# Kernel optimization log

Hardware: AMD Instinct MI355X
Metric: run time of the kernel (lower is better)

## Reference

```python
import jax, jax.numpy as jnp
import numpy as np

S, B, D = 1024, 2, 1024      # seq, batch, embed_dim
E, TOPK = 15, 3              # routed experts = 8*2-1, top_n = 2*2-1
F = 1024                     # per-expert ffn dim (ffn_dim // m)
FS = 2048                    # shared expert ffn dim (ffn_dim * n_shared)


def _uinit(k, shape, out_dim):
    std = out_dim ** -0.5
    return jax.random.uniform(k, shape, jnp.float32, -std, std)


def setup_inputs() -> dict:
    key = jax.random.key(0)
    ks = jax.random.split(key, 10)
    return {
        "x": jax.random.normal(ks[0], (S, B, D), jnp.float32),
        "gate_w": jax.random.normal(ks[1], (E, D), jnp.float32) * (D ** -0.5),
        "fc1_w": _uinit(ks[2], (E, 2 * F, D), 2 * F),
        "fc1_b": _uinit(ks[3], (E, 2 * F), 2 * F),
        "geglu_mult": jnp.ones((E, F), jnp.float32),
        "fc2_w": _uinit(ks[4], (E, D, F), D),
        "fc2_b": _uinit(ks[5], (E, D), D),
        "s_fc1_w": _uinit(ks[6], (2 * FS, D), 2 * FS),
        "s_fc1_b": _uinit(ks[7], (2 * FS,), 2 * FS),
        "s_geglu_mult": jnp.ones((FS,), jnp.float32),
        "s_fc2_w": _uinit(ks[8], (D, FS), D),
        "s_fc2_b": _uinit(ks[9], (D,), D),
    }


def reference(x, gate_w, fc1_w, fc1_b, geglu_mult, fc2_w, fc2_b,
              s_fc1_w, s_fc1_b, s_geglu_mult, s_fc2_w, s_fc2_b):
    s, b, d = x.shape
    xt = x.reshape(-1, d)                              # [T, D] tokens
    T = xt.shape[0]

    # --- gate: softmax over routed experts, top-k, renormalize ---
    logits = xt @ gate_w.T                             # [T, E]
    scores = jax.nn.softmax(logits, axis=-1)
    topk_w, topk_idx = jax.lax.top_k(scores, TOPK)     # [T, K]
    topk_w = topk_w / (jnp.sum(topk_w, axis=-1, keepdims=True) + 1e-20)
    # combine weights: zero for non-routed experts (same math as dispatch/scatter)
    comb = jnp.zeros((T, E), xt.dtype).at[jnp.arange(T)[:, None], topk_idx].add(topk_w)

    # --- routed experts: GEGLU FFN applied as grouped GEMM, weighted combine ---
    h = jnp.einsum('td,efd->etf', xt, fc1_w) + fc1_b[:, None, :]   # [E, T, 2F]
    xh, g = h[..., :F], h[..., F:]                                 # chunk: (x, gate)
    a = jax.nn.gelu(g, approximate=False) * xh * geglu_mult[:, None, :]
    yexp = jnp.einsum('etf,edf->etd', a, fc2_w) + fc2_b[:, None, :]  # [E, T, D]
    y = jnp.einsum('etd,te->td', yexp, comb)                         # [T, D]

    # --- shared expert ---
    hs = xt @ s_fc1_w.T + s_fc1_b                      # [T, 2*FS]
    xs, gs = hs[..., :FS], hs[..., FS:]
    as_ = jax.nn.gelu(gs, approximate=False) * xs * s_geglu_mult
    ys = as_ @ s_fc2_w.T + s_fc2_b                     # [T, D]

    return (y + ys).reshape(s, b, d)
```

## Files before the change

### kernel.cpp

```cpp
#include <hip/hip_runtime.h>

typedef __attribute__((ext_vector_type(8))) short bfrag;
typedef __attribute__((ext_vector_type(4))) float f32x4;

__device__ __forceinline__ short f2bf(float f) {
  union { float f; unsigned u; } v; v.f = f;
  unsigned r = v.u + 0x7FFFu + ((v.u >> 16) & 1u);
  return (short)(r >> 16);
}
__device__ __forceinline__ float bf2f(unsigned short h) {
  union { unsigned u; float f; } v; v.u = ((unsigned)h) << 16;
  return v.f;
}
__device__ __forceinline__ float gelu_exact(float g) {
  return 0.5f * g * (1.0f + erff(g * 0.70710678118654752f));
}
__device__ __forceinline__ void gld_lds16(const short* g, short* l) {
  __builtin_amdgcn_global_load_lds(
      (const __attribute__((address_space(1))) void*)g,
      (__attribute__((address_space(3))) void*)l, 16, 0, 0);
}

__global__ __launch_bounds__(256) void k_convert_w(
    const float* __restrict__ s0, const float* __restrict__ s1,
    const float* __restrict__ s2, const float* __restrict__ s3,
    short* __restrict__ d0, short* __restrict__ d1,
    short* __restrict__ d2, short* __restrict__ d3)
{
  const int b = blockIdx.x;
  const float* s; short* d; long off;
  if (b < 3840)      { s = s0; d = d0; off = (long)b * 2048; }
  else if (b < 5760) { s = s1; d = d1; off = (long)(b - 3840) * 2048; }
  else if (b < 6272) { s = s2; d = d2; off = (long)(b - 5760) * 2048; }
  else               { s = s3; d = d3; off = (long)(b - 6272) * 2048; }
  const f32x4* sp = (const f32x4*)s;
  const long i0 = off + threadIdx.x;
  f32x4 v[8];
#pragma unroll
  for (int j = 0; j < 8; j++) v[j] = __builtin_nontemporal_load(sp + i0 + j * 256);
#pragma unroll
  for (int j = 0; j < 8; j++)
    ((short4*)d)[i0 + j * 256] =
        make_short4(f2bf(v[j].x), f2bf(v[j].y), f2bf(v[j].z), f2bf(v[j].w));
}

__global__ __launch_bounds__(64) void k_gate(const float* __restrict__ x,
    const float* __restrict__ gw, int* __restrict__ topk_idx,
    float* __restrict__ topk_w, short* __restrict__ xbf)
{
  const int t0 = blockIdx.x * 4;
  const int lane = threadIdx.x;
  float xv[4][16];
#pragma unroll
  for (int tt = 0; tt < 4; tt++)
#pragma unroll
    for (int i = 0; i < 16; i++) {
      xv[tt][i] = x[(size_t)(t0 + tt) * 1024 + lane + 64 * i];
      xbf[(size_t)(t0 + tt) * 1024 + lane + 64 * i] = f2bf(xv[tt][i]);
    }
  float p[4][15];
#pragma unroll
  for (int e = 0; e < 15; e++) {
    float wv[16];
#pragma unroll
    for (int i = 0; i < 16; i++) wv[i] = gw[(size_t)e * 1024 + lane + 64 * i];
#pragma unroll
    for (int tt = 0; tt < 4; tt++) {
      float s = 0.f;
#pragma unroll
      for (int i = 0; i < 16; i++) s += xv[tt][i] * wv[i];
#pragma unroll
      for (int o = 32; o; o >>= 1) s += __shfl_xor(s, o, 64);
      p[tt][e] = s;
    }
  }
#pragma unroll
  for (int tt = 0; tt < 4; tt++) {
    float m = -1e30f;
#pragma unroll
    for (int e = 0; e < 15; e++) m = fmaxf(m, p[tt][e]);
    float q[15], Z = 0.f;
#pragma unroll
    for (int e = 0; e < 15; e++) { q[e] = expf(p[tt][e] - m); Z += q[e]; }
    int usedMask = 0; int bi[3]; float bv[3];
#pragma unroll
    for (int j = 0; j < 3; j++) {
      float best = -1.f; int b = 0;
#pragma unroll
      for (int e = 0; e < 15; e++) {
        bool ok = (!((usedMask >> e) & 1)) && (q[e] > best);
        if (ok) { best = q[e]; b = e; }
      }
      bi[j] = b; bv[j] = best / Z; usedMask |= 1 << b;
    }
    if (lane == tt) {
      float den = bv[0] + bv[1] + bv[2] + 1e-20f;
#pragma unroll
      for (int j = 0; j < 3; j++) {
        topk_idx[(t0 + tt) * 3 + j] = bi[j];
        topk_w[(t0 + tt) * 3 + j] = bv[j] / den;
      }
    }
  }
}

__global__ __launch_bounds__(1024) void k_route(const int* __restrict__ topk_idx,
    const float* __restrict__ topk_w, int* __restrict__ cnt_g, int* __restrict__ offs_g,
    int* __restrict__ row_tok, float* __restrict__ row_wt, int* __restrict__ row_id)
{
  __shared__ int scnt[16], soffs[16], sfill[16];
  const int tid = threadIdx.x;
  if (tid < 16) { scnt[tid] = 0; sfill[tid] = 0; }
  __syncthreads();
  for (int i = tid; i < 6144; i += 1024) atomicAdd(&scnt[topk_idx[i]], 1);
  __syncthreads();
  if (tid == 0) {
    int a = 0;
    for (int e = 0; e < 15; e++) { soffs[e] = a; offs_g[e] = a; cnt_g[e] = scnt[e]; a += scnt[e]; }
  }
  __syncthreads();
  for (int i = tid; i < 6144; i += 1024) {
    int e = topk_idx[i];
    int pos = atomicAdd(&sfill[e], 1);
    int row = soffs[e] + pos;
    row_tok[row] = i / 3;
    row_wt[row] = topk_w[i];
    row_id[i] = row;
  }
}

__device__ __forceinline__ bool resolve_tile256(const int* __restrict__ cnt, int ty,
                                                int& e, int& lt) {
  int acc = 0;
#pragma unroll
  for (int i = 0; i < 15; i++) {
    int tl = (cnt[i] + 255) >> 8;
    if (ty < acc + tl) { e = i; lt = ty - acc; return true; }
    acc += tl;
  }
  return false;
}

__global__ __launch_bounds__(512, 2) void k_fc1(
    const short* __restrict__ xbf,
    const short* __restrict__ wsh, const float* __restrict__ bsh, const float* __restrict__ msh,
    const short* __restrict__ wex, const float* __restrict__ bex, const float* __restrict__ mex,
    const int* __restrict__ cnt, const int* __restrict__ offs, const int* __restrict__ row_tok,
    short* __restrict__ as_buf, short* __restrict__ a_buf)
{
  __shared__ short smem[2 * 32768];
  const int tid = threadIdx.x;
  const int bid = blockIdx.x;
  const bool sh = bid < 128;
  int f0, m0 = 0, e = 0, rowBase = 0, nrows = 256;
  if (sh) {
    f0 = (bid & 15) * 128; m0 = (bid >> 4) * 256;
  } else {
    const int b2 = bid - 128;
    int lt;
    if (!resolve_tile256(cnt, b2 >> 3, e, lt)) return;
    f0 = (b2 & 7) * 128;
    rowBase = offs[e] + lt * 256;
    nrows = cnt[e] - lt * 256; if (nrows > 256) nrows = 256;
  }
  const int lane = tid & 63, ml = lane & 15, kq = lane >> 4, mlo = lane & 7;
  const int wv = tid >> 6, wr = wv >> 2, wc = wv & 3;
  const int lrow = lane >> 3, lchk = lane & 7;
  const int Fhalf = sh ? 2048 : 1024;
  const short* wptr = sh ? wsh : (wex + (size_t)e * 2048 * 1024);
  const short* aSrc[4]; const short* bSrc[4];
#pragma unroll
  for (int t = 0; t < 4; t++) {
    const int r = wv * 32 + t * 8 + lrow;
    const int sc = (lchk ^ (r & 7)) * 8;
    if (sh) aSrc[t] = xbf + (size_t)(m0 + r) * 1024 + sc;
    else {
      const int rc = r < nrows ? r : nrows - 1;
      aSrc[t] = xbf + (size_t)row_tok[rowBase + rc] * 1024 + sc;
    }
    const int grow = (r < 128) ? (f0 + r) : (Fhalf + f0 + r - 128);
    bSrc[t] = wptr + (size_t)grow * 1024 + sc;
  }
  f32x4 acc[8][4] = {};

#define FC1_STAGE(BUF, K0) do {                                              \
    short* A_ = smem + (BUF) * 32768;                                        \
    short* B_ = A_ + 16384;                                                  \
    _Pragma("unroll")                                                        \
    for (int t = 0; t < 4; t++) gld_lds16(aSrc[t] + (K0), A_ + (wv * 32 + t * 8) * 64); \
    _Pragma("unroll")                                                        \
    for (int t = 0; t < 4; t++) gld_lds16(bSrc[t] + (K0), B_ + (wv * 32 + t * 8) * 64); \
  } while (0)

#define FC1_COMPUTE(BUF) do {                                                \
    const short* As_ = smem + (BUF) * 32768;                                 \
    const short* Bs_ = As_ + 16384;                                          \
    _Pragma("unroll")                                                        \
    for (int kk = 0; kk < 2; kk++) {                                         \
      const int so = ((kk * 4 + kq) ^ mlo) * 8;                              \
      bfrag af[8], bb[4];                                                    \
      _Pragma("unroll")                                                      \
      for (int i = 0; i < 8; i++)                                            \
        af[i] = *(const bfrag*)&As_[(wr * 128 + i * 16 + ml) * 64 + so];     \
      _Pragma("unroll")                                                      \
      for (int j = 0; j < 4; j++) {                                          \
        const int brow = (j >> 1) * 128 + wc * 32 + (j & 1) * 16 + ml;       \
        bb[j] = *(const bfrag*)&Bs_[brow * 64 + so];                         \
      }                                                                      \
      _Pragma("unroll")                                                      \
      for (int i = 0; i < 8; i++)                                            \
        _Pragma("unroll")                                                    \
        for (int j = 0; j < 4; j++)                                          \
          acc[i][j] = __builtin_amdgcn_mfma_f32_16x16x32_bf16(af[i], bb[j], acc[i][j], 0, 0, 0); \
    }                                                                        \
  } while (0)

  FC1_STAGE(0, 0);
  __syncthreads();
  int cur = 0;
  for (int ks = 0; ks < 15; ks++) {
    FC1_STAGE(cur ^ 1, (ks + 1) * 64);
    FC1_COMPUTE(cur);
    __syncthreads();
    cur ^= 1;
  }
  FC1_COMPUTE(cur);

  const float* bias = sh ? bsh : (bex + (size_t)e * 2048);
  const float* mult = sh ? msh : (mex + (size_t)e * 1024);
#pragma unroll
  for (int jj = 0; jj < 2; jj++) {
    const int fl = wc * 32 + jj * 16 + ml;
    const int f = f0 + fl;
    const float b1 = bias[f];
    const float b2 = bias[Fhalf + f];
    const float mv = mult[f];
#pragma unroll
    for (int i = 0; i < 8; i++)
#pragma unroll
      for (int rg = 0; rg < 4; rg++) {
        const int row = wr * 128 + i * 16 + kq * 4 + rg;
        const float h1 = acc[i][jj][rg] + b1;
        const float h2 = acc[i][jj + 2][rg] + b2;
        const short o = f2bf(gelu_exact(h2) * h1 * mv);
        if (sh) as_buf[(size_t)(m0 + row) * 2048 + f] = o;
        else if (row < nrows) a_buf[(size_t)(rowBase + row) * 1024 + f] = o;
      }
  }
}

__global__ __launch_bounds__(512, 2) void k_fc2(
    const short* __restrict__ as_buf, const short* __restrict__ wsfc2, const float* __restrict__ s_b,
    const short* __restrict__ a_buf, const short* __restrict__ wfc2, const float* __restrict__ e_b,
    const int* __restrict__ cnt, const int* __restrict__ offs, const float* __restrict__ row_wt,
    float* __restrict__ y, short* __restrict__ yexp)
{
  __shared__ short smem[2 * 24576];
  const int tid = threadIdx.x;
  const int bid = blockIdx.x;
  const bool sh = bid < 64;
  int d0, m0 = 0, e = 0, rowBase = 0, nrows = 256, Klen, astr, bstr;
  const short *aBase, *bBase;
  if (sh) {
    d0 = (bid & 7) * 128; m0 = (bid >> 3) * 256;
    Klen = 2048; astr = 2048; bstr = 2048;
    aBase = as_buf; bBase = wsfc2;
  } else {
    const int b2 = bid - 64;
    int lt;
    if (!resolve_tile256(cnt, b2 >> 3, e, lt)) return;
    d0 = (b2 & 7) * 128;
    rowBase = offs[e] + lt * 256;
    nrows = cnt[e] - lt * 256; if (nrows > 256) nrows = 256;
    Klen = 1024; astr = 1024; bstr = 1024;
    aBase = a_buf + (size_t)rowBase * 1024;
    bBase = wfc2 + (size_t)e * 1024 * 1024;
  }
  const int lane = tid & 63, ml = lane & 15, kq = lane >> 4, mlo = lane & 7;
  const int wv = tid >> 6, wr = wv >> 2, wc = wv & 3;
  const int lrow = lane >> 3, lchk = lane & 7;
  const short* aSrc[4]; const short* bSrc[2];
#pragma unroll
  for (int t = 0; t < 4; t++) {
    const int r = wv * 32 + t * 8 + lrow;
    const int sc = (lchk ^ (r & 7)) * 8;
    const int rc = (sh || r < nrows) ? r : nrows - 1;
    aSrc[t] = aBase + (size_t)(sh ? (m0 + r) : rc) * astr + sc;
  }
#pragma unroll
  for (int t = 0; t < 2; t++) {
    const int rb = wv * 16 + t * 8 + lrow;
    const int sc = (lchk ^ (rb & 7)) * 8;
    bSrc[t] = bBase + (size_t)(d0 + rb) * bstr + sc;
  }
  f32x4 acc[8][2] = {};

#define FC2_STAGE(BUF, K0) do {                                              \
    short* A_ = smem + (BUF) * 24576;                                        \
    short* B_ = A_ + 16384;                                                  \
    _Pragma("unroll")                                                        \
    for (int t = 0; t < 4; t++) gld_lds16(aSrc[t] + (K0), A_ + (wv * 32 + t * 8) * 64); \
    _Pragma("unroll")                                                        \
    for (int t = 0; t < 2; t++) gld_lds16(bSrc[t] + (K0), B_ + (wv * 16 + t * 8) * 64); \
  } while (0)

#define FC2_COMPUTE(BUF) do {                                                \
    const short* As_ = smem + (BUF) * 24576;                                 \
    const short* Bs_ = As_ + 16384;                                          \
    _Pragma("unroll")                                                        \
    for (int kk = 0; kk < 2; kk++) {                                         \
      const int so = ((kk * 4 + kq) ^ mlo) * 8;                              \
      bfrag af[8], bb[2];                                                    \
      _Pragma("unroll")                                                      \
      for (int i = 0; i < 8; i++)                                            \
        af[i] = *(const bfrag*)&As_[(wr * 128 + i * 16 + ml) * 64 + so];     \
      _Pragma("unroll")                                                      \
      for (int j = 0; j < 2; j++)                                            \
        bb[j] = *(const bfrag*)&Bs_[(wc * 32 + j * 16 + ml) * 64 + so];      \
      _Pragma("unroll")                                                      \
      for (int i = 0; i < 8; i++)                                            \
        _Pragma("unroll")                                                    \
        for (int j = 0; j < 2; j++)                                          \
          acc[i][j] = __builtin_amdgcn_mfma_f32_16x16x32_bf16(af[i], bb[j], acc[i][j], 0, 0, 0); \
    }                                                                        \
  } while (0)

  FC2_STAGE(0, 0);
  __syncthreads();
  int cur = 0;
  const int NK = Klen >> 6;
  for (int ks = 0; ks < NK - 1; ks++) {
    FC2_STAGE(cur ^ 1, (ks + 1) * 64);
    FC2_COMPUTE(cur);
    __syncthreads();
    cur ^= 1;
  }
  FC2_COMPUTE(cur);

#pragma unroll
  for (int j = 0; j < 2; j++) {
    const int d = d0 + wc * 32 + j * 16 + ml;
    const float bv = sh ? s_b[d] : e_b[(size_t)e * 1024 + d];
#pragma unroll
    for (int i = 0; i < 8; i++)
#pragma unroll
      for (int rg = 0; rg < 4; rg++) {
        const int row = wr * 128 + i * 16 + kq * 4 + rg;
        if (sh) {
          y[(size_t)(m0 + row) * 1024 + d] = acc[i][j][rg] + bv;
        } else if (row < nrows) {
          const float wt = row_wt[rowBase + row];
          yexp[(size_t)(rowBase + row) * 1024 + d] = f2bf((acc[i][j][rg] + bv) * wt);
        }
      }
  }
}

__global__ __launch_bounds__(256) void k_combine(float* __restrict__ y,
    const short* __restrict__ yexp, const int* __restrict__ row_id)
{
  const int idx = blockIdx.x * 256 + threadIdx.x;
  const int t = idx >> 8;
  const int d4 = (idx & 255) * 4;
  const int r0 = row_id[t * 3], r1 = row_id[t * 3 + 1], r2 = row_id[t * 3 + 2];
  float4 acc = *(float4*)(y + (size_t)t * 1024 + d4);
  const ushort4 v0 = *(const ushort4*)(yexp + (size_t)r0 * 1024 + d4);
  const ushort4 v1 = *(const ushort4*)(yexp + (size_t)r1 * 1024 + d4);
  const ushort4 v2 = *(const ushort4*)(yexp + (size_t)r2 * 1024 + d4);
  acc.x += bf2f(v0.x) + bf2f(v1.x) + bf2f(v2.x);
  acc.y += bf2f(v0.y) + bf2f(v1.y) + bf2f(v2.y);
  acc.z += bf2f(v0.z) + bf2f(v1.z) + bf2f(v2.z);
  acc.w += bf2f(v0.w) + bf2f(v1.w) + bf2f(v2.w);
  *(float4*)(y + (size_t)t * 1024 + d4) = acc;
}

extern "C" void kernel_launch(void* const* d_in, const int* in_sizes, int n_in,
                              void* d_out, int out_size, void* d_ws, size_t ws_size,
                              hipStream_t stream) {
  const float* x          = (const float*)d_in[0];
  const float* gate_w     = (const float*)d_in[1];
  const float* fc1_w      = (const float*)d_in[2];
  const float* fc1_b      = (const float*)d_in[3];
  const float* geglu_mult = (const float*)d_in[4];
  const float* fc2_w      = (const float*)d_in[5];
  const float* fc2_b      = (const float*)d_in[6];
  const float* s_fc1_w    = (const float*)d_in[7];
  const float* s_fc1_b    = (const float*)d_in[8];
  const float* s_mult     = (const float*)d_in[9];
  const float* s_fc2_w    = (const float*)d_in[10];
  const float* s_fc2_b    = (const float*)d_in[11];
  float* y = (float*)d_out;

  char* wsb = (char*)d_ws;
  int*   cnt      = (int*)(wsb + 0);
  int*   offs     = (int*)(wsb + 64);
  int*   topk_idx = (int*)(wsb + 256);
  float* topk_w   = (float*)(wsb + 24832);
  int*   row_tok  = (int*)(wsb + 49408);
  float* row_wt   = (float*)(wsb + 74496);
  int*   row_id   = (int*)(wsb + 99584);
  short* xbf      = (short*)(wsb + 131072);
  short* a_buf    = (short*)(wsb + 8519680);
  short* as_buf   = (short*)(wsb + 21364736);
  short* yexp     = (short*)(wsb + 29753344);
  short* wbf_sfc1 = (short*)(wsb + 42598400);
  short* wbf_sfc2 = (short*)(wsb + 50987008);
  short* wbf_fc1  = (short*)(wsb + 55181312);
  short* wbf_fc2  = (short*)(wsb + 118095872);

  k_convert_w<<<6528, 256, 0, stream>>>(fc1_w, fc2_w, s_fc1_w, s_fc2_w,
                                        wbf_fc1, wbf_fc2, wbf_sfc1, wbf_sfc2);
  k_gate<<<512, 64, 0, stream>>>(x, gate_w, topk_idx, topk_w, xbf);
  k_route<<<1, 1024, 0, stream>>>(topk_idx, topk_w, cnt, offs, row_tok, row_wt, row_id);
  k_fc1<<<440, 512, 0, stream>>>(xbf, wbf_sfc1, s_fc1_b, s_mult,
                                 wbf_fc1, fc1_b, geglu_mult,
                                 cnt, offs, row_tok, as_buf, a_buf);
  k_fc2<<<376, 512, 0, stream>>>(as_buf, wbf_sfc2, s_fc2_b,
                                 a_buf, wbf_fc2, fc2_b,
                                 cnt, offs, row_wt, y, yexp);
  k_combine<<<2048, 256, 0, stream>>>(y, yexp, row_id);
}
```

Measured before the change: 416.7 us.

## Use 4-stage BK=32 LDS pipeline with vmcnt waits in fc1/fc2 GEMMs

Both grouped-GEMM kernels change from a double-buffered K=64 tile with a full __syncthreads per step to a four-buffer ring of K=32 tiles with three stages in flight. Waits use explicit s_waitcnt vmcnt counts plus a raw s_barrier, and sched_barrier separates the load issue from the MFMA block. The LDS swizzle is redone for 32-wide rows. The aim is to hide global-to-LDS latency better at the same LDS footprint, at the cost of twice as many barriers and hand-tuned vmcnt values that must match the number of outstanding loads.

```diff
diff --git a/kernel.cpp b/kernel.cpp
--- a/kernel.cpp
+++ b/kernel.cpp
@@ -148,7 +148,7 @@
     const int* __restrict__ cnt, const int* __restrict__ offs, const int* __restrict__ row_tok,
     short* __restrict__ as_buf, short* __restrict__ a_buf)
 {
-  __shared__ short smem[2 * 32768];
+  __shared__ short smem[4 * 16384];
   const int tid = threadIdx.x;
   const int bid = blockIdx.x;
   const bool sh = bid < 128;
@@ -163,68 +163,69 @@
     rowBase = offs[e] + lt * 256;
     nrows = cnt[e] - lt * 256; if (nrows > 256) nrows = 256;
   }
-  const int lane = tid & 63, ml = lane & 15, kq = lane >> 4, mlo = lane & 7;
+  const int lane = tid & 63, ml = lane & 15, kq = lane >> 4;
   const int wv = tid >> 6, wr = wv >> 2, wc = wv & 3;
-  const int lrow = lane >> 3, lchk = lane & 7;
+  const int scol = ((lane & 3) ^ (((lane >> 2) ^ (lane >> 4)) & 3)) * 8;
+  const int so = (kq ^ ((ml ^ (ml >> 2)) & 3)) * 8;
   const int Fhalf = sh ? 2048 : 1024;
   const short* wptr = sh ? wsh : (wex + (size_t)e * 2048 * 1024);
-  const short* aSrc[4]; const short* bSrc[4];
-#pragma unroll
-  for (int t = 0; t < 4; t++) {
-    const int r = wv * 32 + t * 8 + lrow;
-    const int sc = (lchk ^ (r & 7)) * 8;
-    if (sh) aSrc[t] = xbf + (size_t)(m0 + r) * 1024 + sc;
+  const short* aSrc[2]; const short* bSrc[2];
+#pragma unroll
+  for (int t = 0; t < 2; t++) {
+    const int r = wv * 32 + t * 16 + (lane >> 2);
+    if (sh) aSrc[t] = xbf + (size_t)(m0 + r) * 1024 + scol;
     else {
       const int rc = r < nrows ? r : nrows - 1;
-      aSrc[t] = xbf + (size_t)row_tok[rowBase + rc] * 1024 + sc;
+      aSrc[t] = xbf + (size_t)row_tok[rowBase + rc] * 1024 + scol;
     }
     const int grow = (r < 128) ? (f0 + r) : (Fhalf + f0 + r - 128);
-    bSrc[t] = wptr + (size_t)grow * 1024 + sc;
+    bSrc[t] = wptr + (size_t)grow * 1024 + scol;
   }
   f32x4 acc[8][4] = {};
 
 #define FC1_STAGE(BUF, K0) do {                                              \
-    short* A_ = smem + (BUF) * 32768;                                        \
-    short* B_ = A_ + 16384;                                                  \
-    _Pragma("unroll")                                                        \
-    for (int t = 0; t < 4; t++) gld_lds16(aSrc[t] + (K0), A_ + (wv * 32 + t * 8) * 64); \
-    _Pragma("unroll")                                                        \
-    for (int t = 0; t < 4; t++) gld_lds16(bSrc[t] + (K0), B_ + (wv * 32 + t * 8) * 64); \
+    short* A_ = smem + (BUF) * 16384;                                        \
+    short* B_ = A_ + 8192;                                                   \
+    _Pragma("unroll")                                                        \
+    for (int t = 0; t < 2; t++)                                              \
+      gld_lds16(aSrc[t] + (K0), A_ + (wv * 32 + t * 16) * 32);               \
+    _Pragma("unroll")                                                        \
+    for (int t = 0; t < 2; t++)                                              \
+      gld_lds16(bSrc[t] + (K0), B_ + (wv * 32 + t * 16) * 32);               \
   } while (0)
 
 #define FC1_COMPUTE(BUF) do {                                                \
-    const short* As_ = smem + (BUF) * 32768;                                 \
-    const short* Bs_ = As_ + 16384;                                          \
-    _Pragma("unroll")                                                        \
-    for (int kk = 0; kk < 2; kk++) {                                         \
-      const int so = ((kk * 4 + kq) ^ mlo) * 8;                              \
-      bfrag af[8], bb[4];                                                    \
+    const short* As_ = smem + (BUF) * 16384;                                 \
+    const short* Bs_ = As_ + 8192;                                           \
+    bfrag af[8], bb[4];                                                      \
+    _Pragma("unroll")                                                        \
+    for (int i = 0; i < 8; i++)                                              \
+      af[i] = *(const bfrag*)&As_[(wr * 128 + i * 16 + ml) * 32 + so];       \
+    _Pragma("unroll")                                                        \
+    for (int j = 0; j < 4; j++) {                                            \
+      const int brow = (j >> 1) * 128 + wc * 32 + (j & 1) * 16 + ml;         \
+      bb[j] = *(const bfrag*)&Bs_[brow * 32 + so];                           \
+    }                                                                        \
+    _Pragma("unroll")                                                        \
+    for (int i = 0; i < 8; i++)                                              \
       _Pragma("unroll")                                                      \
-      for (int i = 0; i < 8; i++)                                            \
-        af[i] = *(const bfrag*)&As_[(wr * 128 + i * 16 + ml) * 64 + so];     \
-      _Pragma("unroll")                                                      \
-      for (int j = 0; j < 4; j++) {                                          \
-        const int brow = (j >> 1) * 128 + wc * 32 + (j & 1) * 16 + ml;       \
-        bb[j] = *(const bfrag*)&Bs_[brow * 64 + so];                         \
-      }                                                                      \
-      _Pragma("unroll")                                                      \
-      for (int i = 0; i < 8; i++)                                            \
-        _Pragma("unroll")                                                    \
-        for (int j = 0; j < 4; j++)                                          \
-          acc[i][j] = __builtin_amdgcn_mfma_f32_16x16x32_bf16(af[i], bb[j], acc[i][j], 0, 0, 0); \
-    }                                                                        \
+      for (int j = 0; j < 4; j++)                                            \
+        acc[i][j] = __builtin_amdgcn_mfma_f32_16x16x32_bf16(af[i], bb[j], acc[i][j], 0, 0, 0); \
   } while (0)
 
   FC1_STAGE(0, 0);
-  __syncthreads();
-  int cur = 0;
-  for (int ks = 0; ks < 15; ks++) {
-    FC1_STAGE(cur ^ 1, (ks + 1) * 64);
-    FC1_COMPUTE(cur);
-    __syncthreads();
-    cur ^= 1;
-  }
-  FC1_COMPUTE(cur);
+  FC1_STAGE(1, 32);
+  FC1_STAGE(2, 64);
+  for (int ks = 0; ks < 32; ks++) {
+    if (ks < 30)       asm volatile("s_waitcnt vmcnt(8)" ::: "memory");
+    else if (ks == 30) asm volatile("s_waitcnt vmcnt(4)" ::: "memory");
+    else               asm volatile("s_waitcnt vmcnt(0)" ::: "memory");
+    __builtin_amdgcn_s_barrier();
+    __builtin_amdgcn_sched_barrier(0);
+    if (ks + 3 < 32) FC1_STAGE((ks + 3) & 3, (ks + 3) * 32);
+    __builtin_amdgcn_sched_barrier(0);
+    FC1_COMPUTE(ks & 3);
+  }
 
   const float* bias = sh ? bsh : (bex + (size_t)e * 2048);
   const float* mult = sh ? msh : (mex + (size_t)e * 1024);
@@ -255,7 +256,7 @@
     const int* __restrict__ cnt, const int* __restrict__ offs, const float* __restrict__ row_wt,
     float* __restrict__ y, short* __restrict__ yexp)
 {
-  __shared__ short smem[2 * 24576];
+  __shared__ short smem[4 * 12288];
   const int tid = threadIdx.x;
   const int bid = blockIdx.x;
   const bool sh = bid < 64;
@@ -276,66 +277,63 @@
     aBase = a_buf + (size_t)rowBase * 1024;
     bBase = wfc2 + (size_t)e * 1024 * 1024;
   }
-  const int lane = tid & 63, ml = lane & 15, kq = lane >> 4, mlo = lane & 7;
+  const int lane = tid & 63, ml = lane & 15, kq = lane >> 4;
   const int wv = tid >> 6, wr = wv >> 2, wc = wv & 3;
-  const int lrow = lane >> 3, lchk = lane & 7;
-  const short* aSrc[4]; const short* bSrc[2];
-#pragma unroll
-  for (int t = 0; t < 4; t++) {
-    const int r = wv * 32 + t * 8 + lrow;
-    const int sc = (lchk ^ (r & 7)) * 8;
+  const int scol = ((lane & 3) ^ (((lane >> 2) ^ (lane >> 4)) & 3)) * 8;
+  const int so = (kq ^ ((ml ^ (ml >> 2)) & 3)) * 8;
+  const short* aSrc[2]; const short* bSrcP;
+#pragma unroll
+  for (int t = 0; t < 2; t++) {
+    const int r = wv * 32 + t * 16 + (lane >> 2);
     const int rc = (sh || r < nrows) ? r : nrows - 1;
-    aSrc[t] = aBase + (size_t)(sh ? (m0 + r) : rc) * astr + sc;
-  }
-#pragma unroll
-  for (int t = 0; t < 2; t++) {
-    const int rb = wv * 16 + t * 8 + lrow;
-    const int sc = (lchk ^ (rb & 7)) * 8;
-    bSrc[t] = bBase + (size_t)(d0 + rb) * bstr + sc;
+    aSrc[t] = aBase + (size_t)(sh ? (m0 + r) : rc) * astr + scol;
+  }
+  {
+    const int rb = wv * 16 + (lane >> 2);
+    bSrcP = bBase + (size_t)(d0 + rb) * bstr + scol;
   }
   f32x4 acc[8][2] = {};
 
 #define FC2_STAGE(BUF, K0) do {                                              \
-    short* A_ = smem + (BUF) * 24576;                                        \
-    short* B_ = A_ + 16384;                                                  \
-    _Pragma("unroll")                                                        \
-    for (int t = 0; t < 4; t++) gld_lds16(aSrc[t] + (K0), A_ + (wv * 32 + t * 8) * 64); \
-    _Pragma("unroll")                                                        \
-    for (int t = 0; t < 2; t++) gld_lds16(bSrc[t] + (K0), B_ + (wv * 16 + t * 8) * 64); \
+    short* A_ = smem + (BUF) * 12288;                                        \
+    short* B_ = A_ + 8192;                                                   \
+    _Pragma("unroll")                                                        \
+    for (int t = 0; t < 2; t++)                                              \
+      gld_lds16(aSrc[t] + (K0), A_ + (wv * 32 + t * 16) * 32);               \
+    gld_lds16(bSrcP + (K0), B_ + (wv * 16) * 32);                            \
   } while (0)
 
 #define FC2_COMPUTE(BUF) do {                                                \
-    const short* As_ = smem + (BUF) * 24576;                                 \
-    const short* Bs_ = As_ + 16384;                                          \
-    _Pragma("unroll")                                                        \
-    for (int kk = 0; kk < 2; kk++) {                                         \
-      const int so = ((kk * 4 + kq) ^ mlo) * 8;                              \
-      bfrag af[8], bb[2];                                                    \
-      _Pragma("unroll")                                                      \
-      for (int i = 0; i < 8; i++)                                            \
-        af[i] = *(const bfrag*)&As_[(wr * 128 + i * 16 + ml) * 64 + so];     \
+    const short* As_ = smem + (BUF) * 12288;                                 \
+    const short* Bs_ = As_ + 8192;                                           \
+    bfrag af[8], bb[2];                                                      \
+    _Pragma("unroll")                                                        \
+    for (int i = 0; i < 8; i++)                                              \
+      af[i] = *(const bfrag*)&As_[(wr * 128 + i * 16 + ml) * 32 + so];       \
+    _Pragma("unroll")                                                        \
+    for (int j = 0; j < 2; j++)                                              \
+      bb[j] = *(const bfrag*)&Bs_[(wc * 32 + j * 16 + ml) * 32 + so];        \
+    _Pragma("unroll")                                                        \
+    for (int i = 0; i < 8; i++)                                              \
       _Pragma("unroll")                                                      \
       for (int j = 0; j < 2; j++)                                            \
-        bb[j] = *(const bfrag*)&Bs_[(wc * 32 + j * 16 + ml) * 64 + so];      \
-      _Pragma("unroll")                                                      \
-      for (int i = 0; i < 8; i++)                                            \
-        _Pragma("unroll")                                                    \
-        for (int j = 0; j < 2; j++)                                          \
-          acc[i][j] = __builtin_amdgcn_mfma_f32_16x16x32_bf16(af[i], bb[j], acc[i][j], 0, 0, 0); \
-    }                                                                        \
+        acc[i][j] = __builtin_amdgcn_mfma_f32_16x16x32_bf16(af[i], bb[j], acc[i][j], 0, 0, 0); \
   } while (0)
 
   FC2_STAGE(0, 0);
-  __syncthreads();
-  int cur = 0;
-  const int NK = Klen >> 6;
-  for (int ks = 0; ks < NK - 1; ks++) {
-    FC2_STAGE(cur ^ 1, (ks + 1) * 64);
-    FC2_COMPUTE(cur);
-    __syncthreads();
-    cur ^= 1;
-  }
-  FC2_COMPUTE(cur);
+  FC2_STAGE(1, 32);
+  FC2_STAGE(2, 64);
+  const int NK = Klen >> 5;
+  for (int ks = 0; ks < NK; ks++) {
+    if (ks < NK - 2)       asm volatile("s_waitcnt vmcnt(6)" ::: "memory");
+    else if (ks == NK - 2) asm volatile("s_waitcnt vmcnt(3)" ::: "memory");
+    else                   asm volatile("s_waitcnt vmcnt(0)" ::: "memory");
+    __builtin_amdgcn_s_barrier();
+    __builtin_amdgcn_sched_barrier(0);
+    if (ks + 3 < NK) FC2_STAGE((ks + 3) & 3, (ks + 3) * 32);
+    __builtin_amdgcn_sched_barrier(0);
+    FC2_COMPUTE(ks & 3);
+  }
 
 #pragma unroll
   for (int j = 0; j < 2; j++) {
```

New measurement: 428.7 us. 2.9% more time.

## Use partial vmcnt waits to keep next-stage loads in flight during MFMA

Applied to the files above, without the earlier changes.

Restructures the double-buffered main loops of the FC1 and FC2 GEMM kernels. Each iteration now issues the next tile's global-to-LDS loads, then waits only for the previous stage's loads with a partial vmcnt count instead of a full __syncthreads drain. It then computes on the current buffer between raw s_barriers. This lets the prefetch for the following stage overlap the MFMA work. The risk is that the hard-coded vmcnt counts (8 and 6) must exactly match the number of loads each stage issues, or the code reads stale LDS data.

```diff
diff --git a/kernel.cpp b/kernel.cpp
--- a/kernel.cpp
+++ b/kernel.cpp
@@ -216,15 +216,20 @@
   } while (0)
 
   FC1_STAGE(0, 0);
-  __syncthreads();
-  int cur = 0;
-  for (int ks = 0; ks < 15; ks++) {
-    FC1_STAGE(cur ^ 1, (ks + 1) * 64);
-    FC1_COMPUTE(cur);
-    __syncthreads();
-    cur ^= 1;
-  }
-  FC1_COMPUTE(cur);
+  for (int ks = 0; ks < 16; ks++) {
+    if (ks < 15) {
+      FC1_STAGE((ks + 1) & 1, (ks + 1) * 64);
+      asm volatile("s_waitcnt vmcnt(8)" ::: "memory");
+    } else {
+      asm volatile("s_waitcnt vmcnt(0)" ::: "memory");
+    }
+    __builtin_amdgcn_sched_barrier(0);
+    __builtin_amdgcn_s_barrier();
+    __builtin_amdgcn_sched_barrier(0);
+    FC1_COMPUTE(ks & 1);
+    __builtin_amdgcn_s_barrier();
+    __builtin_amdgcn_sched_barrier(0);
+  }
 
   const float* bias = sh ? bsh : (bex + (size_t)e * 2048);
   const float* mult = sh ? msh : (mex + (size_t)e * 1024);
@@ -326,16 +331,21 @@
   } while (0)
 
   FC2_STAGE(0, 0);
-  __syncthreads();
-  int cur = 0;
   const int NK = Klen >> 6;
-  for (int ks = 0; ks < NK - 1; ks++) {
-    FC2_STAGE(cur ^ 1, (ks + 1) * 64);
-    FC2_COMPUTE(cur);
-    __syncthreads();
-    cur ^= 1;
-  }
-  FC2_COMPUTE(cur);
+  for (int ks = 0; ks < NK; ks++) {
+    if (ks < NK - 1) {
+      FC2_STAGE((ks + 1) & 1, (ks + 1) * 64);
+      asm volatile("s_waitcnt vmcnt(6)" ::: "memory");
+    } else {
+      asm volatile("s_waitcnt vmcnt(0)" ::: "memory");
+    }
+    __builtin_amdgcn_sched_barrier(0);
+    __builtin_amdgcn_s_barrier();
+    __builtin_amdgcn_sched_barrier(0);
+    FC2_COMPUTE(ks & 1);
+    __builtin_amdgcn_s_barrier();
+    __builtin_amdgcn_sched_barrier(0);
+  }
 
 #pragma unroll
   for (int j = 0; j < 2; j++) {
```

Measured after the change: 422.9 us. Within noise of the previous version (+1.5%).

## Load GEMM weight fragments straight to registers, bypassing LDS, with register double-buffering

Applied to the files above, without the earlier changes.

In both the fc1 and fc2 grouped GEMM kernels, the B (weight) operand is no longer staged through LDS. Each lane now loads its MFMA fragments directly from global memory into register double buffers, and the K loop is unrolled by two with sched barriers. This halves or shrinks the LDS footprint and removes the LDS reads for B, which could allow more occupancy and less LDS traffic. In exchange it adds register pressure (16 extra bfrag in fc1), makes global loads less coalesced because each lane reads 16 bytes with a row stride, and loses B reuse across the waves that share a column.

```diff
diff --git a/kernel.cpp b/kernel.cpp
--- a/kernel.cpp
+++ b/kernel.cpp
@@ -148,7 +148,7 @@
     const int* __restrict__ cnt, const int* __restrict__ offs, const int* __restrict__ row_tok,
     short* __restrict__ as_buf, short* __restrict__ a_buf)
 {
-  __shared__ short smem[2 * 32768];
+  __shared__ short smem[2 * 16384];
   const int tid = threadIdx.x;
   const int bid = blockIdx.x;
   const bool sh = bid < 128;
@@ -168,7 +168,7 @@
   const int lrow = lane >> 3, lchk = lane & 7;
   const int Fhalf = sh ? 2048 : 1024;
   const short* wptr = sh ? wsh : (wex + (size_t)e * 2048 * 1024);
-  const short* aSrc[4]; const short* bSrc[4];
+  const short* aSrc[4];
 #pragma unroll
   for (int t = 0; t < 4; t++) {
     const int r = wv * 32 + t * 8 + lrow;
@@ -178,53 +178,60 @@
       const int rc = r < nrows ? r : nrows - 1;
       aSrc[t] = xbf + (size_t)row_tok[rowBase + rc] * 1024 + sc;
     }
-    const int grow = (r < 128) ? (f0 + r) : (Fhalf + f0 + r - 128);
-    bSrc[t] = wptr + (size_t)grow * 1024 + sc;
+  }
+  const short* bp[4];
+#pragma unroll
+  for (int j = 0; j < 4; j++) {
+    const int grow = ((j >> 1) ? Fhalf : 0) + f0 + wc * 32 + (j & 1) * 16 + ml;
+    bp[j] = wptr + (size_t)grow * 1024 + kq * 8;
   }
   f32x4 acc[8][4] = {};
-
-#define FC1_STAGE(BUF, K0) do {                                              \
-    short* A_ = smem + (BUF) * 32768;                                        \
-    short* B_ = A_ + 16384;                                                  \
+  bfrag b0[8], b1[8];
+
+#define FC1_ASTAGE(BUF, K0) do {                                             \
+    short* A_ = smem + (BUF) * 16384;                                        \
     _Pragma("unroll")                                                        \
     for (int t = 0; t < 4; t++) gld_lds16(aSrc[t] + (K0), A_ + (wv * 32 + t * 8) * 64); \
-    _Pragma("unroll")                                                        \
-    for (int t = 0; t < 4; t++) gld_lds16(bSrc[t] + (K0), B_ + (wv * 32 + t * 8) * 64); \
-  } while (0)
-
-#define FC1_COMPUTE(BUF) do {                                                \
-    const short* As_ = smem + (BUF) * 32768;                                 \
-    const short* Bs_ = As_ + 16384;                                          \
+  } while (0)
+
+#define FC1_BLOAD(BB, K0) do {                                               \
+    _Pragma("unroll")                                                        \
+    for (int kk = 0; kk < 2; kk++)                                           \
+      _Pragma("unroll")                                                      \
+      for (int j = 0; j < 4; j++)                                            \
+        BB[kk * 4 + j] = *(const bfrag*)(bp[j] + (K0) + kk * 32);            \
+  } while (0)
+
+#define FC1_COMPUTE(BUF, BB) do {                                            \
+    const short* As_ = smem + (BUF) * 16384;                                 \
     _Pragma("unroll")                                                        \
     for (int kk = 0; kk < 2; kk++) {                                         \
       const int so = ((kk * 4 + kq) ^ mlo) * 8;                              \
-      bfrag af[8], bb[4];                                                    \
+      bfrag af[8];                                                           \
       _Pragma("unroll")                                                      \
       for (int i = 0; i < 8; i++)                                            \
         af[i] = *(const bfrag*)&As_[(wr * 128 + i * 16 + ml) * 64 + so];     \
-      _Pragma("unroll")                                                      \
-      for (int j = 0; j < 4; j++) {                                          \
-        const int brow = (j >> 1) * 128 + wc * 32 + (j & 1) * 16 + ml;       \
-        bb[j] = *(const bfrag*)&Bs_[brow * 64 + so];                         \
-      }                                                                      \
       _Pragma("unroll")                                                      \
       for (int i = 0; i < 8; i++)                                            \
         _Pragma("unroll")                                                    \
         for (int j = 0; j < 4; j++)                                          \
-          acc[i][j] = __builtin_amdgcn_mfma_f32_16x16x32_bf16(af[i], bb[j], acc[i][j], 0, 0, 0); \
+          acc[i][j] = __builtin_amdgcn_mfma_f32_16x16x32_bf16(af[i], BB[kk * 4 + j], acc[i][j], 0, 0, 0); \
     }                                                                        \
   } while (0)
 
-  FC1_STAGE(0, 0);
+  FC1_ASTAGE(0, 0);
+  FC1_BLOAD(b0, 0);
   __syncthreads();
-  int cur = 0;
-  for (int ks = 0; ks < 15; ks++) {
-    FC1_STAGE(cur ^ 1, (ks + 1) * 64);
-    FC1_COMPUTE(cur);
+  for (int ks = 0; ks < 16; ks += 2) {
+    if (ks < 15) { FC1_ASTAGE(1, (ks + 1) * 64); FC1_BLOAD(b1, (ks + 1) * 64); }
+    __builtin_amdgcn_sched_barrier(0);
+    FC1_COMPUTE(0, b0);
     __syncthreads();
-    cur ^= 1;
-  }
-  FC1_COMPUTE(cur);
+    if (ks + 2 < 16) { FC1_ASTAGE(0, (ks + 2) * 64); FC1_BLOAD(b0, (ks + 2) * 64); }
+    __builtin_amdgcn_sched_barrier(0);
+    FC1_COMPUTE(1, b1);
+    __syncthreads();
+  }
 
   const float* bias = sh ? bsh : (bex + (size_t)e * 2048);
   const float* mult = sh ? msh : (mex + (size_t)e * 1024);
@@ -232,16 +239,16 @@
   for (int jj = 0; jj < 2; jj++) {
     const int fl = wc * 32 + jj * 16 + ml;
     const int f = f0 + fl;
-    const float b1 = bias[f];
-    const float b2 = bias[Fhalf + f];
+    const float b1v = bias[f];
+    const float b2v = bias[Fhalf + f];
     const float mv = mult[f];
 #pragma unroll
     for (int i = 0; i < 8; i++)
 #pragma unroll
       for (int rg = 0; rg < 4; rg++) {
         const int row = wr * 128 + i * 16 + kq * 4 + rg;
-        const float h1 = acc[i][jj][rg] + b1;
-        const float h2 = acc[i][jj + 2][rg] + b2;
+        const float h1 = acc[i][jj][rg] + b1v;
+        const float h2 = acc[i][jj + 2][rg] + b2v;
         const short o = f2bf(gelu_exact(h2) * h1 * mv);
         if (sh) as_buf[(size_t)(m0 + row) * 2048 + f] = o;
         else if (row < nrows) a_buf[(size_t)(rowBase + row) * 1024 + f] = o;
@@ -255,7 +262,7 @@
     const int* __restrict__ cnt, const int* __restrict__ offs, const float* __restrict__ row_wt,
     float* __restrict__ y, short* __restrict__ yexp)
 {
-  __shared__ short smem[2 * 24576];
+  __shared__ short smem[2 * 16384];
   const int tid = threadIdx.x;
   const int bid = blockIdx.x;
   const bool sh = bid < 64;
@@ -279,7 +286,7 @@
   const int lane = tid & 63, ml = lane & 15, kq = lane >> 4, mlo = lane & 7;
   const int wv = tid >> 6, wr = wv >> 2, wc = wv & 3;
   const int lrow = lane >> 3, lchk = lane & 7;
-  const short* aSrc[4]; const short* bSrc[2];
+  const short* aSrc[4];
 #pragma unroll
   for (int t = 0; t < 4; t++) {
     const int r = wv * 32 + t * 8 + lrow;
@@ -287,55 +294,60 @@
     const int rc = (sh || r < nrows) ? r : nrows - 1;
     aSrc[t] = aBase + (size_t)(sh ? (m0 + r) : rc) * astr + sc;
   }
-#pragma unroll
-  for (int t = 0; t < 2; t++) {
-    const int rb = wv * 16 + t * 8 + lrow;
-    const int sc = (lchk ^ (rb & 7)) * 8;
-    bSrc[t] = bBase + (size_t)(d0 + rb) * bstr + sc;
+  const short* bp[2];
+#pragma unroll
+  for (int j = 0; j < 2; j++) {
+    const int grow = d0 + wc * 32 + j * 16 + ml;
+    bp[j] = bBase + (size_t)grow * bstr + kq * 8;
   }
   f32x4 acc[8][2] = {};
-
-#define FC2_STAGE(BUF, K0) do {                                              \
-    short* A_ = smem + (BUF) * 24576;                                        \
-    short* B_ = A_ + 16384;                                                  \
+  bfrag b0[4], b1[4];
+
+#define FC2_ASTAGE(BUF, K0) do {                                             \
+    short* A_ = smem + (BUF) * 16384;                                        \
     _Pragma("unroll")                                                        \
     for (int t = 0; t < 4; t++) gld_lds16(aSrc[t] + (K0), A_ + (wv * 32 + t * 8) * 64); \
-    _Pragma("unroll")                                                        \
-    for (int t = 0; t < 2; t++) gld_lds16(bSrc[t] + (K0), B_ + (wv * 16 + t * 8) * 64); \
-  } while (0)
-
-#define FC2_COMPUTE(BUF) do {                                                \
-    const short* As_ = smem + (BUF) * 24576;                                 \
-    const short* Bs_ = As_ + 16384;                                          \
+  } while (0)
+
+#define FC2_BLOAD(BB, K0) do {                                               \
+    _Pragma("unroll")                                                        \
+    for (int kk = 0; kk < 2; kk++)                                           \
+      _Pragma("unroll")                                                      \
+      for (int j = 0; j < 2; j++)                                            \
+        BB[kk * 2 + j] = *(const bfrag*)(bp[j] + (K0) + kk * 32);            \
+  } while (0)
+
+#define FC2_COMPUTE(BUF, BB) do {                                            \
+    const short* As_ = smem + (BUF) * 16384;                                 \
     _Pragma("unroll")                                                        \
     for (int kk = 0; kk < 2; kk++) {                                         \
       const int so = ((kk * 4 + kq) ^ mlo) * 8;                              \
-      bfrag af[8], bb[2];                                                    \
+      bfrag af[8];                                                           \
       _Pragma("unroll")                                                      \
       for (int i = 0; i < 8; i++)                                            \
         af[i] = *(const bfrag*)&As_[(wr * 128 + i * 16 + ml) * 64 + so];     \
-      _Pragma("unroll")                                                      \
-      for (int j = 0; j < 2; j++)                                            \
-        bb[j] = *(const bfrag*)&Bs_[(wc * 32 + j * 16 + ml) * 64 + so];      \
       _Pragma("unroll")                                                      \
       for (int i = 0; i < 8; i++)                                            \
         _Pragma("unroll")                                                    \
         for (int j = 0; j < 2; j++)                                          \
-          acc[i][j] = __builtin_amdgcn_mfma_f32_16x16x32_bf16(af[i], bb[j], acc[i][j], 0, 0, 0); \
+          acc[i][j] = __builtin_amdgcn_mfma_f32_16x16x32_bf16(af[i], BB[kk * 2 + j], acc[i][j], 0, 0, 0); \
     }                                                                        \
   } while (0)
 
-  FC2_STAGE(0, 0);
+  FC2_ASTAGE(0, 0);
+  FC2_BLOAD(b0, 0);
   __syncthreads();
-  int cur = 0;
   const int NK = Klen >> 6;
-  for (int ks = 0; ks < NK - 1; ks++) {
-    FC2_STAGE(cur ^ 1, (ks + 1) * 64);
-    FC2_COMPUTE(cur);
+  for (int ks = 0; ks < NK; ks += 2) {
+    if (ks + 1 < NK) { FC2_ASTAGE(1, (ks + 1) * 64); FC2_BLOAD(b1, (ks + 1) * 64); }
+    __builtin_amdgcn_sched_barrier(0);
+    FC2_COMPUTE(0, b0);
     __syncthreads();
-    cur ^= 1;
-  }
-  FC2_COMPUTE(cur);
+    if (ks + 2 < NK) { FC2_ASTAGE(0, (ks + 2) * 64); FC2_BLOAD(b0, (ks + 2) * 64); }
+    __builtin_amdgcn_sched_barrier(0);
+    FC2_COMPUTE(1, b1);
+    __syncthreads();
+  }
 
 #pragma unroll
   for (int j = 0; j < 2; j++) {
```

Measured after the change: 515.0 us. 23.6% more time.
